# Kernel optimization log

Hardware: AMD Instinct MI355X
Metric: run time of the kernel (lower is better)

## Reference

```python
import jax, jax.numpy as jnp
import numpy as np

B, H, S = 32, 128, 8192

def setup_inputs() -> dict:
    key = jax.random.key(0)
    k1, k2, k3, k4, k5 = jax.random.split(key, 5)
    return {
        "static_hidden": jax.random.normal(k1, (B, H, S), dtype=jnp.float32),
        "dynamic_hidden": jax.random.normal(k2, (B, H, S), dtype=jnp.float32),
        "decoder_hidden": jax.random.normal(k3, (B, H), dtype=jnp.float32),
        "v": jax.random.normal(k4, (1, 1, H), dtype=jnp.float32) * 0.01,
        "W": jax.random.normal(k5, (1, H, 3 * H), dtype=jnp.float32) * 0.01,
    }

def reference(static_hidden, dynamic_hidden, decoder_hidden, v, W):
    b, h, s = static_hidden.shape
    # concat (static, dynamic, expanded decoder) along feature dim -> [b, 3h, s]
    hidden = jnp.concatenate(
        [static_hidden, dynamic_hidden,
         jnp.broadcast_to(decoder_hidden[:, :, None], (b, h, s))], axis=1)
    # W[0]: [h, 3h]; tanh(W @ hidden) -> [b, h, s]
    e = jnp.tanh(jnp.einsum('hk,bks->bhs', W[0], hidden))
    # v[0,0]: [h]; scores -> [b, 1, s]
    scores = jnp.einsum('h,bhs->bs', v[0, 0], e)[:, None, :]
    return jax.nn.softmax(scores, axis=2)
```

## Files before the change

### kernel.cpp

```cpp
#include <hip/hip_runtime.h>
#include <math.h>

#define BB 32
#define HH 128
#define SS 8192

typedef __attribute__((ext_vector_type(8))) short bf8;
typedef __attribute__((ext_vector_type(4))) float f4;

static __device__ __forceinline__ unsigned short f2bf(float x) {
  union { float f; unsigned int u; } c; c.f = x;
  unsigned int r = c.u + 0x7FFFu + ((c.u >> 16) & 1u);
  return (unsigned short)(r >> 16);
}

__global__ __launch_bounds__(256) void prep_kernel(
    const float* __restrict__ W, const float* __restrict__ dec,
    unsigned short* __restrict__ Abf, float* __restrict__ bias) {
  const int b = blockIdx.x;
  const int tid = threadIdx.x;
  if (tid < HH) {
    const float* wr = W + (size_t)tid * 384 + 256;
    const float* db = dec + (size_t)b * HH;
    float acc = 0.f;
    #pragma unroll 8
    for (int j = 0; j < HH; ++j) acc += wr[j] * db[j];
    bias[b * HH + tid] = acc;
  }
  if (b == 0) {
    for (int idx = tid; idx < HH * 256; idx += 256) {
      int h = idx >> 8, k = idx & 255;
      Abf[idx] = f2bf(W[h * 384 + k]);
    }
  }
}

__global__ __launch_bounds__(1024, 4) void attn_main(
    const float* __restrict__ sta, const float* __restrict__ dyn,
    const unsigned short* __restrict__ Abf, const float* __restrict__ bias,
    const float* __restrict__ v, float* __restrict__ scores) {
  extern __shared__ __align__(16) unsigned short smem[];
  unsigned short* LA = smem;
  unsigned short* LX = smem + 32768;

  const int tid  = threadIdx.x;
  const int l    = tid & 63;
  const int w    = tid >> 6;
  const int quad = l >> 4;
  const int n16  = l & 15;
  const int b     = blockIdx.x >> 5;
  const int s_blk = (blockIdx.x & 31) << 8;

  const int kq = ((w >> 2) << 4) + (quad << 2);
  const int sl = ((w & 3) << 6) + (n16 << 2);
  const size_t gxoff = ((size_t)b * HH) * SS + s_blk + sl;

  f4 g[4];
  auto issueX = [&](int c) {
    const float* p = (c < 2 ? sta : dyn) + gxoff + (size_t)(((c & 1) << 6) + kq) * SS;
    #pragma unroll
    for (int j = 0; j < 4; ++j) g[j] = *(const f4*)(p + (size_t)j * SS);
  };
  auto convWrite = [&](int buf) {
    unsigned short* X = LX + (buf << 14);
    #pragma unroll
    for (int i = 0; i < 4; ++i) {
      const int srow = sl + i;
      ushort4 o;
      o.x = f2bf(g[0][i]); o.y = f2bf(g[1][i]);
      o.z = f2bf(g[2][i]); o.w = f2bf(g[3][i]);
      *(ushort4*)&X[(srow << 6) + ((((kq >> 3) ^ (srow & 7)) << 3) | (kq & 7))] = o;
    }
  };

  issueX(0);
  #pragma unroll
  for (int j = 0; j < 4; ++j) {
    int gc = (j << 10) + tid;
    int m = gc >> 5, ck = gc & 31;
    bf8 val = *(const bf8*)(Abf + ((size_t)gc << 3));
    *(bf8*)&LA[(m << 8) + ((ck ^ (m & 7)) << 3)] = val;
  }
  convWrite(0);
  __syncthreads();

  f4 acc[8];
  #pragma unroll
  for (int mt = 0; mt < 8; ++mt) acc[mt] = (f4){0.f, 0.f, 0.f, 0.f};

  const int srow = (w << 4) + n16;
  const int xrow = srow << 6;
  const int sswz = srow & 7;
  const int aswz = n16 & 7;

  #pragma unroll
  for (int c = 0; c < 4; ++c) {
    if (c < 3) issueX(c + 1);
    const unsigned short* X = LX + ((c & 1) << 14);
    bf8 bf0 = *(const bf8*)&X[xrow + ((quad ^ sswz) << 3)];
    bf8 bf1 = *(const bf8*)&X[xrow + (((4 + quad) ^ sswz) << 3)];
    #pragma unroll
    for (int mt = 0; mt < 8; ++mt) {
      const int arow = (mt << 4) + n16;
      bf8 a0 = *(const bf8*)&LA[(arow << 8) + ((((c << 3) + quad) ^ aswz) << 3)];
      acc[mt] = __builtin_amdgcn_mfma_f32_16x16x32_bf16(a0, bf0, acc[mt], 0, 0, 0);
      bf8 a1 = *(const bf8*)&LA[(arow << 8) + ((((c << 3) + 4 + quad) ^ aswz) << 3)];
      acc[mt] = __builtin_amdgcn_mfma_f32_16x16x32_bf16(a1, bf1, acc[mt], 0, 0, 0);
    }
    if (c < 3) convWrite((c + 1) & 1);
    __syncthreads();
  }

  float part = 0.f;
  #pragma unroll
  for (int mt = 0; mt < 8; ++mt) {
    #pragma unroll
    for (int r = 0; r < 4; ++r) {
      const int h = (mt << 4) + (quad << 2) + r;
      part += v[h] * tanhf(acc[mt][r] + bias[(b << 7) + h]);
    }
  }
  part += __shfl_xor(part, 16, 64);
  part += __shfl_xor(part, 32, 64);
  if (quad == 0)
    scores[((size_t)b << 13) + s_blk + srow] = part;
}

__global__ __launch_bounds__(1024) void softmax_kernel(float* __restrict__ out) {
  const int b = blockIdx.x;
  const int tid = threadIdx.x;
  float* row = out + ((size_t)b << 13);
  float4 x0 = ((const float4*)row)[tid];
  float4 x1 = ((const float4*)row)[tid + 1024];
  float lmax = fmaxf(fmaxf(fmaxf(x0.x, x0.y), fmaxf(x0.z, x0.w)),
                     fmaxf(fmaxf(x1.x, x1.y), fmaxf(x1.z, x1.w)));
  __shared__ float red[17];
  #pragma unroll
  for (int o = 32; o >= 1; o >>= 1) lmax = fmaxf(lmax, __shfl_xor(lmax, o, 64));
  if ((tid & 63) == 0) red[tid >> 6] = lmax;
  __syncthreads();
  if (tid < 64) {
    float m = (tid < 16) ? red[tid] : -3.0e38f;
    #pragma unroll
    for (int o = 8; o >= 1; o >>= 1) m = fmaxf(m, __shfl_xor(m, o, 64));
    if (tid == 0) red[16] = m;
  }
  __syncthreads();
  const float gmax = red[16];
  float e[8];
  e[0] = expf(x0.x - gmax); e[1] = expf(x0.y - gmax);
  e[2] = expf(x0.z - gmax); e[3] = expf(x0.w - gmax);
  e[4] = expf(x1.x - gmax); e[5] = expf(x1.y - gmax);
  e[6] = expf(x1.z - gmax); e[7] = expf(x1.w - gmax);
  float ls = e[0] + e[1] + e[2] + e[3] + e[4] + e[5] + e[6] + e[7];
  #pragma unroll
  for (int o = 32; o >= 1; o >>= 1) ls += __shfl_xor(ls, o, 64);
  __syncthreads();
  if ((tid & 63) == 0) red[tid >> 6] = ls;
  __syncthreads();
  if (tid < 64) {
    float m = (tid < 16) ? red[tid] : 0.f;
    #pragma unroll
    for (int o = 8; o >= 1; o >>= 1) m += __shfl_xor(m, o, 64);
    if (tid == 0) red[16] = m;
  }
  __syncthreads();
  const float inv = 1.0f / red[16];
  float4 o0 = make_float4(e[0] * inv, e[1] * inv, e[2] * inv, e[3] * inv);
  float4 o1 = make_float4(e[4] * inv, e[5] * inv, e[6] * inv, e[7] * inv);
  ((float4*)row)[tid] = o0;
  ((float4*)row)[tid + 1024] = o1;
}

extern "C" void kernel_launch(void* const* d_in, const int* in_sizes, int n_in,
                              void* d_out, int out_size, void* d_ws, size_t ws_size,
                              hipStream_t stream) {
  const float* sta = (const float*)d_in[0];
  const float* dyn = (const float*)d_in[1];
  const float* dec = (const float*)d_in[2];
  const float* v   = (const float*)d_in[3];
  const float* W   = (const float*)d_in[4];

  unsigned short* Abf = (unsigned short*)d_ws;
  float* bias = (float*)((char*)d_ws + 128 * 256 * 2);
  float* scores = (float*)d_out;

  static bool attr_done = false;
  if (!attr_done) {
    (void)hipFuncSetAttribute((const void*)attn_main,
                              hipFuncAttributeMaxDynamicSharedMemorySize, 131072);
    attr_done = true;
  }

  prep_kernel<<<BB, 256, 0, stream>>>(W, dec, Abf, bias);
  attn_main<<<BB * 32, 1024, 131072, stream>>>(sta, dyn, Abf, bias, v, scores);
  softmax_kernel<<<BB, 1024, 0, stream>>>(scores);
}
```

Before: 327.6 us.

## Make attention blocks persistent over four S-strips with two-deep prefetch

Each block now processes four 256-column strips of S instead of one, cutting the grid from 1024 to 256 blocks. The 64KB bf16 W tile is loaded into LDS once per block and reused across all four strips. Global loads run two stages ahead through double-buffered registers, so the memory stream continues across strip boundaries. The X swizzle also changes, to avoid LDS bank conflicts. In exchange, a grid of 256 blocks on a chip with 256 CUs gives one block per CU with little occupancy slack, and the extra prefetch buffer adds register pressure.

```diff
diff --git a/kernel.cpp b/kernel.cpp
--- a/kernel.cpp
+++ b/kernel.cpp
@@ -13,6 +13,8 @@
   unsigned int r = c.u + 0x7FFFu + ((c.u >> 16) & 1u);
   return (unsigned short)(r >> 16);
 }
+
+#define XSWZ(r) ((((r) >> 2) ^ (r)) & 7)
 
 __global__ __launch_bounds__(256) void prep_kernel(
     const float* __restrict__ W, const float* __restrict__ dec,
@@ -28,6 +30,7 @@
     bias[b * HH + tid] = acc;
   }
   if (b == 0) {
+    #pragma unroll 4
     for (int idx = tid; idx < HH * 256; idx += 256) {
       int h = idx >> 8, k = idx & 255;
       Abf[idx] = f2bf(W[h * 384 + k]);
@@ -48,32 +51,36 @@
   const int w    = tid >> 6;
   const int quad = l >> 4;
   const int n16  = l & 15;
-  const int b     = blockIdx.x >> 5;
-  const int s_blk = (blockIdx.x & 31) << 8;
+  const int b       = blockIdx.x >> 3;
+  const int sb_base = (blockIdx.x & 7) << 2;
 
   const int kq = ((w >> 2) << 4) + (quad << 2);
   const int sl = ((w & 3) << 6) + (n16 << 2);
-  const size_t gxoff = ((size_t)b * HH) * SS + s_blk + sl;
-
-  f4 g[4];
-  auto issueX = [&](int c) {
-    const float* p = (c < 2 ? sta : dyn) + gxoff + (size_t)(((c & 1) << 6) + kq) * SS;
-    #pragma unroll
-    for (int j = 0; j < 4; ++j) g[j] = *(const f4*)(p + (size_t)j * SS);
+  const size_t xoff_b = (size_t)b * HH * SS;
+
+  f4 g[2][4];
+
+  auto issueX = [&](int t, f4* gg) {
+    const int c = t & 3;
+    const float* base = (c < 2) ? sta : dyn;
+    const float* p = base + xoff_b + (size_t)(((c & 1) << 6) + kq) * SS
+                   + (((sb_base + (t >> 2)) << 8) + sl);
+    #pragma unroll
+    for (int j = 0; j < 4; ++j) gg[j] = *(const f4*)(p + (size_t)j * SS);
   };
-  auto convWrite = [&](int buf) {
+  auto convWrite = [&](const f4* gg, int buf) {
     unsigned short* X = LX + (buf << 14);
     #pragma unroll
     for (int i = 0; i < 4; ++i) {
       const int srow = sl + i;
       ushort4 o;
-      o.x = f2bf(g[0][i]); o.y = f2bf(g[1][i]);
-      o.z = f2bf(g[2][i]); o.w = f2bf(g[3][i]);
-      *(ushort4*)&X[(srow << 6) + ((((kq >> 3) ^ (srow & 7)) << 3) | (kq & 7))] = o;
+      o.x = f2bf(gg[0][i]); o.y = f2bf(gg[1][i]);
+      o.z = f2bf(gg[2][i]); o.w = f2bf(gg[3][i]);
+      *(ushort4*)&X[(srow << 6) + ((((kq >> 3) ^ XSWZ(srow)) << 3) | (kq & 7))] = o;
     }
   };
 
-  issueX(0);
+  issueX(0, g[0]);
   #pragma unroll
   for (int j = 0; j < 4; ++j) {
     int gc = (j << 10) + tid;
@@ -81,49 +88,55 @@
     bf8 val = *(const bf8*)(Abf + ((size_t)gc << 3));
     *(bf8*)&LA[(m << 8) + ((ck ^ (m & 7)) << 3)] = val;
   }
-  convWrite(0);
+  issueX(1, g[1]);
+  convWrite(g[0], 0);
   __syncthreads();
 
   f4 acc[8];
   #pragma unroll
   for (int mt = 0; mt < 8; ++mt) acc[mt] = (f4){0.f, 0.f, 0.f, 0.f};
 
-  const int srow = (w << 4) + n16;
-  const int xrow = srow << 6;
-  const int sswz = srow & 7;
+  const int srow_f = (w << 4) + n16;
+  const int xrow = srow_f << 6;
+  const int sswz = XSWZ(srow_f);
   const int aswz = n16 & 7;
 
-  #pragma unroll
-  for (int c = 0; c < 4; ++c) {
-    if (c < 3) issueX(c + 1);
-    const unsigned short* X = LX + ((c & 1) << 14);
-    bf8 bf0 = *(const bf8*)&X[xrow + ((quad ^ sswz) << 3)];
-    bf8 bf1 = *(const bf8*)&X[xrow + (((4 + quad) ^ sswz) << 3)];
-    #pragma unroll
-    for (int mt = 0; mt < 8; ++mt) {
-      const int arow = (mt << 4) + n16;
-      bf8 a0 = *(const bf8*)&LA[(arow << 8) + ((((c << 3) + quad) ^ aswz) << 3)];
-      acc[mt] = __builtin_amdgcn_mfma_f32_16x16x32_bf16(a0, bf0, acc[mt], 0, 0, 0);
-      bf8 a1 = *(const bf8*)&LA[(arow << 8) + ((((c << 3) + 4 + quad) ^ aswz) << 3)];
-      acc[mt] = __builtin_amdgcn_mfma_f32_16x16x32_bf16(a1, bf1, acc[mt], 0, 0, 0);
+  for (int strip = 0; strip < 4; ++strip) {
+    #pragma unroll
+    for (int c = 0; c < 4; ++c) {
+      const int t = (strip << 2) + c;
+      if (t + 2 < 16) issueX(t + 2, g[c & 1]);
+      const unsigned short* X = LX + ((c & 1) << 14);
+      bf8 bf0 = *(const bf8*)&X[xrow + ((quad ^ sswz) << 3)];
+      bf8 bf1 = *(const bf8*)&X[xrow + (((4 + quad) ^ sswz) << 3)];
+      #pragma unroll
+      for (int mt = 0; mt < 8; ++mt) {
+        const int arow = (mt << 4) + n16;
+        bf8 a0 = *(const bf8*)&LA[(arow << 8) + ((((c << 3) + quad) ^ aswz) << 3)];
+        acc[mt] = __builtin_amdgcn_mfma_f32_16x16x32_bf16(a0, bf0, acc[mt], 0, 0, 0);
+        bf8 a1 = *(const bf8*)&LA[(arow << 8) + ((((c << 3) + 4 + quad) ^ aswz) << 3)];
+        acc[mt] = __builtin_amdgcn_mfma_f32_16x16x32_bf16(a1, bf1, acc[mt], 0, 0, 0);
+      }
+      if (t + 1 < 16) convWrite(g[(c + 1) & 1], (c + 1) & 1);
+      if (c == 3) {
+        float part = 0.f;
+        #pragma unroll
+        for (int mt = 0; mt < 8; ++mt) {
+          #pragma unroll
+          for (int r = 0; r < 4; ++r) {
+            const int h = (mt << 4) + (quad << 2) + r;
+            part += v[h] * tanhf(acc[mt][r] + bias[(b << 7) + h]);
+            acc[mt][r] = 0.f;
+          }
+        }
+        part += __shfl_xor(part, 16, 64);
+        part += __shfl_xor(part, 32, 64);
+        if (quad == 0)
+          scores[((size_t)b << 13) + (((sb_base + strip) << 8) + srow_f)] = part;
+      }
+      __syncthreads();
     }
-    if (c < 3) convWrite((c + 1) & 1);
-    __syncthreads();
-  }
-
-  float part = 0.f;
-  #pragma unroll
-  for (int mt = 0; mt < 8; ++mt) {
-    #pragma unroll
-    for (int r = 0; r < 4; ++r) {
-      const int h = (mt << 4) + (quad << 2) + r;
-      part += v[h] * tanhf(acc[mt][r] + bias[(b << 7) + h]);
-    }
-  }
-  part += __shfl_xor(part, 16, 64);
-  part += __shfl_xor(part, 32, 64);
-  if (quad == 0)
-    scores[((size_t)b << 13) + s_blk + srow] = part;
+  }
 }
 
 __global__ __launch_bounds__(1024) void softmax_kernel(float* __restrict__ out) {
@@ -193,6 +206,6 @@
   }
 
   prep_kernel<<<BB, 256, 0, stream>>>(W, dec, Abf, bias);
-  attn_main<<<BB * 32, 1024, 131072, stream>>>(sta, dyn, Abf, bias, v, scores);
+  attn_main<<<BB * 8, 1024, 131072, stream>>>(sta, dyn, Abf, bias, v, scores);
   softmax_kernel<<<BB, 1024, 0, stream>>>(scores);
 }
```

Result: slower. 385.5 us (+17.7%).
